# Kernel optimization log

Hardware: AMD Instinct MI355X
Metric: run time of the kernel (lower is better)

## Reference

```python
import jax, jax.numpy as jnp
import numpy as np

N_NODES = 100000
N_EDGES = 600000
N_GRAPHS = 256
HID = 128
IN_DIM = 7
POCKET_DIM = 28
BN_EPS = 1e-5


def setup_inputs() -> dict:
    key = jax.random.key(0)
    ks = jax.random.split(key, 24)
    d = {}
    d['x'] = jax.random.normal(ks[0], (N_NODES, IN_DIM), dtype=jnp.float32)
    d['edge_index'] = jax.random.randint(ks[1], (2, N_EDGES), 0, N_NODES, dtype=jnp.int32)
    d['batch'] = jnp.sort(jax.random.randint(ks[2], (N_NODES,), 0, N_GRAPHS, dtype=jnp.int32))
    d['pocket'] = jax.random.normal(ks[3], (POCKET_DIM,), dtype=jnp.float32)
    # GCN layer weights (PyG GCNConv: lin then normalized aggregation, bias after)
    def glorot(k, shape):
        lim = np.sqrt(6.0 / (shape[0] + shape[1]))
        return jax.random.uniform(k, shape, jnp.float32, -lim, lim)
    d['W0'] = glorot(ks[4], (IN_DIM, HID)); d['b0'] = jnp.zeros((HID,), jnp.float32)
    d['W1'] = glorot(ks[5], (HID, HID)); d['b1'] = jnp.zeros((HID,), jnp.float32)
    d['W2'] = glorot(ks[6], (HID, HID)); d['b2'] = jnp.zeros((HID,), jnp.float32)
    # BatchNorm (eval mode) params for 3 layers
    d['bn_gamma'] = jax.random.uniform(ks[7], (3, HID), jnp.float32, 0.5, 1.5)
    d['bn_beta'] = 0.1 * jax.random.normal(ks[8], (3, HID), dtype=jnp.float32)
    d['bn_mean'] = 0.1 * jax.random.normal(ks[9], (3, HID), dtype=jnp.float32)
    d['bn_var'] = jax.random.uniform(ks[10], (3, HID), jnp.float32, 0.5, 1.5)
    # pocket MLP: 28 -> 64 -> 64
    d['pw1'] = glorot(ks[11], (POCKET_DIM, 64)); d['pb1'] = jnp.zeros((64,), jnp.float32)
    d['pw2'] = glorot(ks[12], (64, 64)); d['pb2'] = jnp.zeros((64,), jnp.float32)
    # classifier: 192 -> 96 -> 1
    d['cw1'] = glorot(ks[13], (HID + 64, 96)); d['cb1'] = jnp.zeros((96,), jnp.float32)
    d['cw2'] = glorot(ks[14], (96, 1)); d['cb2'] = jnp.zeros((1,), jnp.float32)
    return d


def reference(x, edge_index, batch, pocket, W0, b0, W1, b1, W2, b2,
              bn_gamma, bn_beta, bn_mean, bn_var,
              pw1, pb1, pw2, pb2, cw1, cb1, cw2, cb2):
    src, dst = edge_index[0], edge_index[1]
    n = x.shape[0]
    # degree with self-loops (GCNConv default add_self_loops=True)
    deg = jax.ops.segment_sum(jnp.ones((src.shape[0],), x.dtype), dst, num_segments=n) + 1.0
    dinv = jax.lax.rsqrt(deg)                      # [N]
    norm = dinv[src] * dinv[dst]                   # [E] edge normalization
    self_norm = (dinv * dinv)[:, None]             # [N,1] self-loop norm

    h = x
    for i, (W, b) in enumerate(((W0, b0), (W1, b1), (W2, b2))):
        hl = h @ W                                  # [N,HID]
        agg = jax.ops.segment_sum(hl[src] * norm[:, None], dst, num_segments=n)
        agg = agg + hl * self_norm + b
        # BatchNorm1d in eval mode with running stats
        bn = (agg - bn_mean[i]) * (bn_gamma[i] * jax.lax.rsqrt(bn_var[i] + BN_EPS)) + bn_beta[i]
        h = jax.nn.relu(bn)                         # dropout is identity in eval

    # global mean pool over graphs
    sums = jax.ops.segment_sum(h, batch, num_segments=N_GRAPHS)          # [B,HID]
    cnts = jax.ops.segment_sum(jnp.ones((n,), h.dtype), batch, num_segments=N_GRAPHS)
    lig = sums / jnp.maximum(cnts, 1.0)[:, None]

    # pocket MLP, broadcast to batch
    p = jax.nn.relu(pocket @ pw1 + pb1) @ pw2 + pb2                      # [64]
    pe = jnp.broadcast_to(p[None, :], (N_GRAPHS, 64))

    emb = jnp.concatenate([lig, pe], axis=1)                             # [B,192]
    logits = (jax.nn.relu(emb @ cw1 + cb1) @ cw2 + cb2)[:, 0]            # [B]
    return logits
```

## Files before the change

### kernel.cpp

```cpp
#include <hip/hip_runtime.h>

#define NN 100000
#define NE 600000
#define NG 256
#define HID 128
#define BN_EPS 1e-5f

#define SCAN_TILE 1024
#define NTILES ((NN + SCAN_TILE - 1) / SCAN_TILE)
#define MM_TILES (NN / 32)

typedef __attribute__((ext_vector_type(8))) short short8;
typedef __attribute__((ext_vector_type(4))) float float4v;

__device__ __forceinline__ unsigned short f2bf_rn(float f) {
    unsigned u = __float_as_uint(f);
    unsigned r = u + 0x7FFFu + ((u >> 16) & 1u);
    return (unsigned short)(r >> 16);
}
__device__ __forceinline__ float bf2f(unsigned short h) {
    return __uint_as_float((unsigned)h << 16);
}
__device__ __forceinline__ void unpack8(uint4 u, float* f) {
    f[0] = __uint_as_float(u.x << 16); f[1] = __uint_as_float(u.x & 0xFFFF0000u);
    f[2] = __uint_as_float(u.y << 16); f[3] = __uint_as_float(u.y & 0xFFFF0000u);
    f[4] = __uint_as_float(u.z << 16); f[5] = __uint_as_float(u.z & 0xFFFF0000u);
    f[6] = __uint_as_float(u.w << 16); f[7] = __uint_as_float(u.w & 0xFFFF0000u);
}


__global__ __launch_bounds__(256) void hist_kernel(const int* __restrict__ dst, int* __restrict__ cnt) {
    int e = blockIdx.x * blockDim.x + threadIdx.x;
    if (e < NE) atomicAdd(&cnt[dst[e]], 1);
}


__global__ __launch_bounds__(256) void scan_a(const int* __restrict__ cnt, int* __restrict__ rs,
                                              int* __restrict__ tsum, float* __restrict__ dinv) {
    __shared__ int s[256];
    int t = threadIdx.x;
    int base = blockIdx.x * SCAN_TILE;
    int idx = base + t * 4;
    int v0 = (idx + 0 < NN) ? cnt[idx + 0] : 0;
    int v1 = (idx + 1 < NN) ? cnt[idx + 1] : 0;
    int v2 = (idx + 2 < NN) ? cnt[idx + 2] : 0;
    int v3 = (idx + 3 < NN) ? cnt[idx + 3] : 0;
    if (idx + 0 < NN) dinv[idx + 0] = rsqrtf((float)v0 + 1.0f);
    if (idx + 1 < NN) dinv[idx + 1] = rsqrtf((float)v1 + 1.0f);
    if (idx + 2 < NN) dinv[idx + 2] = rsqrtf((float)v2 + 1.0f);
    if (idx + 3 < NN) dinv[idx + 3] = rsqrtf((float)v3 + 1.0f);
    int local = v0 + v1 + v2 + v3;
    s[t] = local;
    __syncthreads();
    for (int off = 1; off < 256; off <<= 1) {
        int x = (t >= off) ? s[t - off] : 0;
        __syncthreads();
        s[t] += x;
        __syncthreads();
    }
    int pre = s[t] - local;
    if (t == 255) tsum[blockIdx.x] = s[255];
    if (idx + 0 < NN) rs[idx + 0] = pre; pre += v0;
    if (idx + 1 < NN) rs[idx + 1] = pre; pre += v1;
    if (idx + 2 < NN) rs[idx + 2] = pre; pre += v2;
    if (idx + 3 < NN) rs[idx + 3] = pre;
}

__global__ __launch_bounds__(128) void scan_b(int* __restrict__ tsum) {
    __shared__ int s[128];
    int t = threadIdx.x;
    int v = (t < NTILES) ? tsum[t] : 0;
    s[t] = v;
    __syncthreads();
    for (int off = 1; off < 128; off <<= 1) {
        int x = (t >= off) ? s[t - off] : 0;
        __syncthreads();
        s[t] += x;
        __syncthreads();
    }
    if (t < NTILES) tsum[t] = s[t] - v;
}

__global__ __launch_bounds__(256) void scan_c(int* __restrict__ rs, const int* __restrict__ tsum,
                                              int* __restrict__ cursor) {
    int t = threadIdx.x;
    int base = blockIdx.x * SCAN_TILE;
    int off = tsum[blockIdx.x];
    for (int k = 0; k < 4; k++) {
        int idx = base + t * 4 + k;
        if (idx < NN) {
            int v = rs[idx] + off;
            rs[idx] = v;
            cursor[idx] = v;
        }
    }
    if (blockIdx.x == 0 && t == 0) rs[NN] = NE;
}


__global__ __launch_bounds__(256) void bucket_prep_kernel(const int* __restrict__ src, const int* __restrict__ dst,
                                                          int* __restrict__ cursor, int* __restrict__ esrc,
                                                          const float* __restrict__ W1, const float* __restrict__ W2,
                                                          unsigned short* __restrict__ w1hi, unsigned short* __restrict__ w1lo,
                                                          unsigned short* __restrict__ w2hi, unsigned short* __restrict__ w2lo,
                                                          const float* __restrict__ pocket,
                                                          const float* __restrict__ pw1, const float* __restrict__ pb1,
                                                          const float* __restrict__ pw2, const float* __restrict__ pb2,
                                                          float* __restrict__ pv, int nb) {
    if ((int)blockIdx.x < nb) {
        int e = blockIdx.x * 256 + threadIdx.x;
        if (e < NE) {
            int pos = atomicAdd(&cursor[dst[e]], 1);
            esrc[pos] = src[e];
        }
    } else if ((int)blockIdx.x < nb + 64) {
        int t = (blockIdx.x - nb) * 256 + threadIdx.x;
        int k = t >> 7, n = t & 127;
        int to = n * HID + k;
        float v1 = W1[t];
        unsigned short h1 = f2bf_rn(v1);
        w1hi[to] = h1;
        w1lo[to] = f2bf_rn(v1 - bf2f(h1));
        float v2 = W2[t];
        unsigned short h2 = f2bf_rn(v2);
        w2hi[to] = h2;
        w2lo[to] = f2bf_rn(v2 - bf2f(h2));
    } else {
        __shared__ float t1[64];
        int j = threadIdx.x;
        if (j < 64) {
            float acc = pb1[j];
            for (int k = 0; k < 28; k++) acc = fmaf(pocket[k], pw1[k * 64 + j], acc);
            t1[j] = fmaxf(acc, 0.f);
        }
        __syncthreads();
        if (j < 64) {
            float acc2 = pb2[j];
            for (int k = 0; k < 64; k++) acc2 = fmaf(t1[k], pw2[k * 64 + j], acc2);
            pv[j] = acc2;
        }
    }
}


__global__ __launch_bounds__(256) void l0_fused(const float* __restrict__ x,
                                                const int* __restrict__ rs,
                                                const int* __restrict__ esrc,
                                                const float* __restrict__ dinv,
                                                const float* __restrict__ W,
                                                const float* __restrict__ b,
                                                const float* __restrict__ gamma,
                                                const float* __restrict__ beta,
                                                const float* __restrict__ mean,
                                                const float* __restrict__ var,
                                                unsigned short* __restrict__ ohi) {
    int c4 = threadIdx.x & 31;
    int r8 = threadIdx.x >> 5;
    float w[7][4];
#pragma unroll
    for (int k = 0; k < 7; k++)
#pragma unroll
        for (int i = 0; i < 4; i++) w[k][i] = W[k * HID + c4 * 4 + i];
    float4 bb = ((const float4*)b)[c4];
    float4 ga = ((const float4*)gamma)[c4];
    float4 be = ((const float4*)beta)[c4];
    float4 me = ((const float4*)mean)[c4];
    float4 va = ((const float4*)var)[c4];
    float4 sc;
    sc.x = ga.x * rsqrtf(va.x + BN_EPS);
    sc.y = ga.y * rsqrtf(va.y + BN_EPS);
    sc.z = ga.z * rsqrtf(va.z + BN_EPS);
    sc.w = ga.w * rsqrtf(va.w + BN_EPS);
    int m = threadIdx.x >> 3, f = threadIdx.x & 7;
    __shared__ float s[32][8];
    int n0 = blockIdx.x * 32;
    float acc = 0.f;
    int n = n0 + m;
    if (f < 7) {
        float di = dinv[n];
        acc = x[n * 7 + f] * di * di;
        int e0 = rs[n], e1 = rs[n + 1];
        int e = e0;
        for (; e + 1 < e1; e += 2) {
            int s0 = esrc[e], s1 = esrc[e + 1];
            float w0 = dinv[s0] * di, w1 = dinv[s1] * di;
            float a0 = x[s0 * 7 + f];
            float a1 = x[s1 * 7 + f];
            acc = fmaf(a0, w0, acc);
            acc = fmaf(a1, w1, acc);
        }
        if (e < e1) {
            int s0 = esrc[e];
            acc = fmaf(x[s0 * 7 + f], dinv[s0] * di, acc);
        }
    }
    s[m][f] = acc;
    __syncthreads();
#pragma unroll
    for (int g = 0; g < 4; g++) {
        int m2 = g * 8 + r8;
        float o0 = bb.x, o1 = bb.y, o2 = bb.z, o3 = bb.w;
#pragma unroll
        for (int k = 0; k < 7; k++) {
            float xv = s[m2][k];
            o0 = fmaf(xv, w[k][0], o0);
            o1 = fmaf(xv, w[k][1], o1);
            o2 = fmaf(xv, w[k][2], o2);
            o3 = fmaf(xv, w[k][3], o3);
        }
        ushort4 hi4;
        hi4.x = f2bf_rn(fmaxf(fmaf(o0 - me.x, sc.x, be.x), 0.f));
        hi4.y = f2bf_rn(fmaxf(fmaf(o1 - me.y, sc.y, be.y), 0.f));
        hi4.z = f2bf_rn(fmaxf(fmaf(o2 - me.z, sc.z, be.z), 0.f));
        hi4.w = f2bf_rn(fmaxf(fmaf(o3 - me.w, sc.w, be.w), 0.f));
        *(ushort4*)(ohi + (size_t)(n0 + m2) * HID + c4 * 4) = hi4;
    }
}


__global__ __launch_bounds__(256) void mm_mfma(const unsigned short* __restrict__ A,
                                               const unsigned short* __restrict__ Whi,
                                               const unsigned short* __restrict__ Wlo,
                                               unsigned short* __restrict__ out) {
    int wave = threadIdx.x >> 6;
    int lane = threadIdx.x & 63;
    int mrow = lane & 15;
    int quad = lane >> 4;
    int n0 = wave * 32;

    short8 bh[2][4], bl[2][4];
#pragma unroll
    for (int ct = 0; ct < 2; ct++) {
#pragma unroll
        for (int kc = 0; kc < 4; kc++) {
            size_t off = (size_t)(n0 + ct * 16 + mrow) * HID + kc * 32 + quad * 8;
            bh[ct][kc] = *(const short8*)(Whi + off);
            bl[ct][kc] = *(const short8*)(Wlo + off);
        }
    }

    int tile = blockIdx.x;
    if (tile >= MM_TILES) return;

    short8 ah[2][4];
#pragma unroll
    for (int rt = 0; rt < 2; rt++)
#pragma unroll
        for (int kc = 0; kc < 4; kc++)
            ah[rt][kc] = *(const short8*)(A + (size_t)(tile * 32 + rt * 16 + mrow) * HID + kc * 32 + quad * 8);

    for (;;) {
        int nt = tile + gridDim.x;
        bool has_next = nt < MM_TILES;
        short8 an[2][4];
        if (has_next) {
#pragma unroll
            for (int rt = 0; rt < 2; rt++)
#pragma unroll
                for (int kc = 0; kc < 4; kc++)
                    an[rt][kc] = *(const short8*)(A + (size_t)(nt * 32 + rt * 16 + mrow) * HID + kc * 32 + quad * 8);
        }

        float4v acc[2][2];
#pragma unroll
        for (int rt = 0; rt < 2; rt++)
#pragma unroll
            for (int ct = 0; ct < 2; ct++) {
                acc[rt][ct].x = 0.f; acc[rt][ct].y = 0.f;
                acc[rt][ct].z = 0.f; acc[rt][ct].w = 0.f;
            }

#pragma unroll
        for (int kc = 0; kc < 4; kc++)
#pragma unroll
            for (int rt = 0; rt < 2; rt++)
#pragma unroll
                for (int ct = 0; ct < 2; ct++) {
                    acc[rt][ct] = __builtin_amdgcn_mfma_f32_16x16x32_bf16(ah[rt][kc], bh[ct][kc], acc[rt][ct], 0, 0, 0);
                    acc[rt][ct] = __builtin_amdgcn_mfma_f32_16x16x32_bf16(ah[rt][kc], bl[ct][kc], acc[rt][ct], 0, 0, 0);
                }

        int m0 = tile * 32;
#pragma unroll
        for (int rt = 0; rt < 2; rt++)
#pragma unroll
            for (int ct = 0; ct < 2; ct++) {
                int col = n0 + ct * 16 + mrow;
#pragma unroll
                for (int r = 0; r < 4; r++) {
                    int row = m0 + rt * 16 + quad * 4 + r;
                    out[(size_t)row * HID + col] = f2bf_rn(acc[rt][ct][r]);
                }
            }

        if (!has_next) break;
#pragma unroll
        for (int rt = 0; rt < 2; rt++)
#pragma unroll
            for (int kc = 0; kc < 4; kc++) ah[rt][kc] = an[rt][kc];
        tile = nt;
    }
}


__global__ __launch_bounds__(256) void gather_bn(const unsigned short* __restrict__ hl,
                                                 const int* __restrict__ rs,
                                                 const int* __restrict__ esrc,
                                                 const float* __restrict__ dinv,
                                                 const float* __restrict__ b,
                                                 const float* __restrict__ gamma,
                                                 const float* __restrict__ beta,
                                                 const float* __restrict__ mean,
                                                 const float* __restrict__ var,
                                                 unsigned short* __restrict__ ohi) {
    int t = blockIdx.x * blockDim.x + threadIdx.x;
    int lane = t & 15;
    int n = t >> 4;
    if (n >= NN) return;
    const uint4* hlv = (const uint4*)hl;
    float di = dinv[n];
    float dsq = di * di;

    float acc[8], v[8];
    {
        uint4 sv = hlv[(size_t)n * 16 + lane];
        unpack8(sv, v);
        float4 bA = ((const float4*)b)[lane * 2];
        float4 bB = ((const float4*)b)[lane * 2 + 1];
        acc[0] = fmaf(v[0], dsq, bA.x); acc[1] = fmaf(v[1], dsq, bA.y);
        acc[2] = fmaf(v[2], dsq, bA.z); acc[3] = fmaf(v[3], dsq, bA.w);
        acc[4] = fmaf(v[4], dsq, bB.x); acc[5] = fmaf(v[5], dsq, bB.y);
        acc[6] = fmaf(v[6], dsq, bB.z); acc[7] = fmaf(v[7], dsq, bB.w);
    }

    int e0 = rs[n], e1 = rs[n + 1];
    int e = e0;
    for (; e + 3 < e1; e += 4) {
        int s0 = esrc[e], s1 = esrc[e + 1], s2 = esrc[e + 2], s3 = esrc[e + 3];
        float w0 = dinv[s0] * di, w1 = dinv[s1] * di;
        float w2 = dinv[s2] * di, w3 = dinv[s3] * di;
        uint4 u0 = hlv[(size_t)s0 * 16 + lane];
        uint4 u1 = hlv[(size_t)s1 * 16 + lane];
        uint4 u2 = hlv[(size_t)s2 * 16 + lane];
        uint4 u3 = hlv[(size_t)s3 * 16 + lane];
        unpack8(u0, v);
#pragma unroll
        for (int i = 0; i < 8; i++) acc[i] = fmaf(v[i], w0, acc[i]);
        unpack8(u1, v);
#pragma unroll
        for (int i = 0; i < 8; i++) acc[i] = fmaf(v[i], w1, acc[i]);
        unpack8(u2, v);
#pragma unroll
        for (int i = 0; i < 8; i++) acc[i] = fmaf(v[i], w2, acc[i]);
        unpack8(u3, v);
#pragma unroll
        for (int i = 0; i < 8; i++) acc[i] = fmaf(v[i], w3, acc[i]);
    }
    for (; e < e1; e++) {
        int s0 = esrc[e];
        float w0 = dinv[s0] * di;
        uint4 u0 = hlv[(size_t)s0 * 16 + lane];
        unpack8(u0, v);
#pragma unroll
        for (int i = 0; i < 8; i++) acc[i] = fmaf(v[i], w0, acc[i]);
    }

    float4 gA = ((const float4*)gamma)[lane * 2], gB = ((const float4*)gamma)[lane * 2 + 1];
    float4 eA = ((const float4*)beta)[lane * 2],  eB = ((const float4*)beta)[lane * 2 + 1];
    float4 mA = ((const float4*)mean)[lane * 2],  mB = ((const float4*)mean)[lane * 2 + 1];
    float4 vA = ((const float4*)var)[lane * 2],   vB = ((const float4*)var)[lane * 2 + 1];
    float o[8];
    o[0] = fmaxf(fmaf(acc[0] - mA.x, gA.x * rsqrtf(vA.x + BN_EPS), eA.x), 0.f);
    o[1] = fmaxf(fmaf(acc[1] - mA.y, gA.y * rsqrtf(vA.y + BN_EPS), eA.y), 0.f);
    o[2] = fmaxf(fmaf(acc[2] - mA.z, gA.z * rsqrtf(vA.z + BN_EPS), eA.z), 0.f);
    o[3] = fmaxf(fmaf(acc[3] - mA.w, gA.w * rsqrtf(vA.w + BN_EPS), eA.w), 0.f);
    o[4] = fmaxf(fmaf(acc[4] - mB.x, gB.x * rsqrtf(vB.x + BN_EPS), eB.x), 0.f);
    o[5] = fmaxf(fmaf(acc[5] - mB.y, gB.y * rsqrtf(vB.y + BN_EPS), eB.y), 0.f);
    o[6] = fmaxf(fmaf(acc[6] - mB.z, gB.z * rsqrtf(vB.z + BN_EPS), eB.z), 0.f);
    o[7] = fmaxf(fmaf(acc[7] - mB.w, gB.w * rsqrtf(vB.w + BN_EPS), eB.w), 0.f);

    uint4 p;
    p.x = (unsigned)f2bf_rn(o[0]) | ((unsigned)f2bf_rn(o[1]) << 16);
    p.y = (unsigned)f2bf_rn(o[2]) | ((unsigned)f2bf_rn(o[3]) << 16);
    p.z = (unsigned)f2bf_rn(o[4]) | ((unsigned)f2bf_rn(o[5]) << 16);
    p.w = (unsigned)f2bf_rn(o[6]) | ((unsigned)f2bf_rn(o[7]) << 16);
    ((uint4*)ohi)[(size_t)n * 16 + lane] = p;
}


__global__ __launch_bounds__(1024) void poolcls_kernel(const unsigned short* __restrict__ h,
                                                       const int* __restrict__ batch,
                                                       const float* __restrict__ pv,
                                                       const float* __restrict__ cw1,
                                                       const float* __restrict__ cb1,
                                                       const float* __restrict__ cw2,
                                                       const float* __restrict__ cb2,
                                                       float* __restrict__ out) {
    int g = blockIdx.x;
    int lane = threadIdx.x & 31;
    int row = threadIdx.x >> 5;
    __shared__ int se[2];
    __shared__ float emb[192];
    __shared__ float hid[96];
    if (threadIdx.x < 2) {
        int target = g + threadIdx.x;
        int lo = 0, hi = NN;
        while (lo < hi) {
            int mid = (lo + hi) >> 1;
            if (batch[mid] < target) lo = mid + 1; else hi = mid;
        }
        se[threadIdx.x] = lo;
    }
    if (threadIdx.x < 64) emb[128 + threadIdx.x] = pv[threadIdx.x];
    __syncthreads();
    int start = se[0], end = se[1];
    const uint2* h2 = (const uint2*)h;
    float4 acc = make_float4(0.f, 0.f, 0.f, 0.f);
    for (int n = start + row; n < end; n += 32) {
        uint2 u = h2[(size_t)n * 32 + lane];
        acc.x += __uint_as_float(u.x << 16);
        acc.y += __uint_as_float(u.x & 0xFFFF0000u);
        acc.z += __uint_as_float(u.y << 16);
        acc.w += __uint_as_float(u.y & 0xFFFF0000u);
    }
    __shared__ float4 part[32][32];
    part[row][lane] = acc;
    __syncthreads();
#pragma unroll
    for (int off = 16; off >= 1; off >>= 1) {
        if (row < off) {
            float4 a = part[row][lane];
            float4 c = part[row + off][lane];
            a.x += c.x; a.y += c.y; a.z += c.z; a.w += c.w;
            part[row][lane] = a;
        }
        __syncthreads();
    }
    if (row == 0) {
        float inv = 1.0f / fmaxf((float)(end - start), 1.0f);
        float4 a = part[0][lane];
        a.x *= inv; a.y *= inv; a.z *= inv; a.w *= inv;
        ((float4*)emb)[lane] = a;
    }
    __syncthreads();
    int j = threadIdx.x;
    if (j < 96) {
        float a = cb1[j];
        for (int k = 0; k < 192; k++) a = fmaf(emb[k], cw1[k * 96 + j], a);
        hid[j] = fmaxf(a, 0.f) * cw2[j];
    }
    __syncthreads();
    if (j == 0) {
        float s = cb2[0];
        for (int k = 0; k < 96; k++) s += hid[k];
        out[g] = s;
    }
}

extern "C" void kernel_launch(void* const* d_in, const int* in_sizes, int n_in,
                              void* d_out, int out_size, void* d_ws, size_t ws_size,
                              hipStream_t stream) {
    const float* x        = (const float*)d_in[0];
    const int*   eidx     = (const int*)d_in[1];
    const int*   batch    = (const int*)d_in[2];
    const float* pocket   = (const float*)d_in[3];
    const float* W0 = (const float*)d_in[4];
    const float* b0 = (const float*)d_in[5];
    const float* W1 = (const float*)d_in[6];
    const float* b1 = (const float*)d_in[7];
    const float* W2 = (const float*)d_in[8];
    const float* b2 = (const float*)d_in[9];
    const float* bn_gamma = (const float*)d_in[10];
    const float* bn_beta  = (const float*)d_in[11];
    const float* bn_mean  = (const float*)d_in[12];
    const float* bn_var   = (const float*)d_in[13];
    const float* pw1 = (const float*)d_in[14]; const float* pb1 = (const float*)d_in[15];
    const float* pw2 = (const float*)d_in[16]; const float* pb2 = (const float*)d_in[17];
    const float* cw1 = (const float*)d_in[18]; const float* cb1 = (const float*)d_in[19];
    const float* cw2 = (const float*)d_in[20]; const float* cb2 = (const float*)d_in[21];
    float* out = (float*)d_out;

    float* ws   = (float*)d_ws;
    float* dinv = ws;
    int*   cnt  = (int*)(ws + NN);
    int*   rs   = cnt + NN;
    int*   tsum = rs + NN + 1;
    int*   esrc = tsum + 128;
    unsigned short* w1hi = (unsigned short*)(esrc + NE);
    unsigned short* w1lo = w1hi + HID * HID;
    unsigned short* w2hi = w1lo + HID * HID;
    unsigned short* w2lo = w2hi + HID * HID;
    size_t head = (size_t)NN * 2 + (NN + 1) + 128 + NE + (4 * HID * HID) / 2;
    head = (head + 3) & ~(size_t)3;
    unsigned short* A = (unsigned short*)(ws + head);
    unsigned short* B = A + (size_t)NN * HID;
    float* pv   = (float*)(B + (size_t)NN * HID);

    const int* srcp = eidx;
    const int* dstp = eidx + NE;

    const int NB = (NE + 255) / 256;

    hipMemsetAsync(cnt, 0, NN * sizeof(int), stream);
    hist_kernel<<<NB, 256, 0, stream>>>(dstp, cnt);
    scan_a<<<NTILES, 256, 0, stream>>>(cnt, rs, tsum, dinv);
    scan_b<<<1, 128, 0, stream>>>(tsum);
    scan_c<<<NTILES, 256, 0, stream>>>(rs, tsum, cnt);
    bucket_prep_kernel<<<NB + 65, 256, 0, stream>>>(srcp, dstp, cnt, esrc,
                                                    W1, W2, w1hi, w1lo, w2hi, w2lo,
                                                    pocket, pw1, pb1, pw2, pb2, pv, NB);

    l0_fused<<<MM_TILES, 256, 0, stream>>>(x, rs, esrc, dinv, W0, b0,
                                           bn_gamma + 0 * HID, bn_beta + 0 * HID,
                                           bn_mean + 0 * HID, bn_var + 0 * HID, A);

    const int MM_BLOCKS = 1024;
    const int GA_BLOCKS = (NN * 16 + 255) / 256;

    mm_mfma<<<MM_BLOCKS, 256, 0, stream>>>(A, w1hi, w1lo, B);
    gather_bn<<<GA_BLOCKS, 256, 0, stream>>>(
        B, rs, esrc, dinv, b1,
        bn_gamma + 1 * HID, bn_beta + 1 * HID, bn_mean + 1 * HID, bn_var + 1 * HID, A);
    mm_mfma<<<MM_BLOCKS, 256, 0, stream>>>(A, w2hi, w2lo, B);
    gather_bn<<<GA_BLOCKS, 256, 0, stream>>>(
        B, rs, esrc, dinv, b2,
        bn_gamma + 2 * HID, bn_beta + 2 * HID, bn_mean + 2 * HID, bn_var + 2 * HID, A);

    poolcls_kernel<<<NG, 1024, 0, stream>>>(A, batch, pv, cw1, cb1, cw2, cb2, out);
}
```

Measured before the change: 334.0 us.

## Sort CSR neighbor lists and order nodes by degree; fold tile scan into scan_c

Adds a degree histogram in scan_a and a degree-bucketed node permutation in scan_c. The separate single-block tile-offset scan is dropped: each scan_c block reduces the earlier tile sums itself. A new kernel uses that permutation to insertion-sort each node's source list, so neighboring threads handle nodes of similar degree. Sorted sources are meant to make the gathers in the aggregation kernels more cache-friendly and deterministic, at the cost of an extra kernel, a wider memset, and extra atomics in the scans.

```diff
diff --git a/kernel.cpp b/kernel.cpp
--- a/kernel.cpp
+++ b/kernel.cpp
@@ -36,8 +36,10 @@
 
 
 __global__ __launch_bounds__(256) void scan_a(const int* __restrict__ cnt, int* __restrict__ rs,
-                                              int* __restrict__ tsum, float* __restrict__ dinv) {
+                                              int* __restrict__ tsum, float* __restrict__ dinv,
+                                              int* __restrict__ dbin) {
     __shared__ int s[256];
+    __shared__ int hb[64];
     int t = threadIdx.x;
     int base = blockIdx.x * SCAN_TILE;
     int idx = base + t * 4;
@@ -51,7 +53,12 @@
     if (idx + 3 < NN) dinv[idx + 3] = rsqrtf((float)v3 + 1.0f);
     int local = v0 + v1 + v2 + v3;
     s[t] = local;
-    __syncthreads();
+    if (t < 64) hb[t] = 0;
+    __syncthreads();
+    if (idx + 0 < NN) atomicAdd(&hb[v0 < 63 ? v0 : 63], 1);
+    if (idx + 1 < NN) atomicAdd(&hb[v1 < 63 ? v1 : 63], 1);
+    if (idx + 2 < NN) atomicAdd(&hb[v2 < 63 ? v2 : 63], 1);
+    if (idx + 3 < NN) atomicAdd(&hb[v3 < 63 ? v3 : 63], 1);
     for (int off = 1; off < 256; off <<= 1) {
         int x = (t >= off) ? s[t - off] : 0;
         __syncthreads();
@@ -60,38 +67,59 @@
     }
     int pre = s[t] - local;
     if (t == 255) tsum[blockIdx.x] = s[255];
+    if (t < 64 && hb[t]) atomicAdd(&dbin[t], hb[t]);
     if (idx + 0 < NN) rs[idx + 0] = pre; pre += v0;
     if (idx + 1 < NN) rs[idx + 1] = pre; pre += v1;
     if (idx + 2 < NN) rs[idx + 2] = pre; pre += v2;
     if (idx + 3 < NN) rs[idx + 3] = pre;
 }
 
-__global__ __launch_bounds__(128) void scan_b(int* __restrict__ tsum) {
-    __shared__ int s[128];
+
+__global__ __launch_bounds__(256) void scan_c(int* __restrict__ rs, const int* __restrict__ tsum,
+                                              int* __restrict__ cursor, const int* __restrict__ dbin,
+                                              int* __restrict__ dcur, int* __restrict__ perm) {
+    __shared__ int s[256];
+    __shared__ int pb[64];
+    __shared__ int lb[64];
     int t = threadIdx.x;
-    int v = (t < NTILES) ? tsum[t] : 0;
-    s[t] = v;
-    __syncthreads();
-    for (int off = 1; off < 128; off <<= 1) {
-        int x = (t >= off) ? s[t - off] : 0;
-        __syncthreads();
-        s[t] += x;
-        __syncthreads();
-    }
-    if (t < NTILES) tsum[t] = s[t] - v;
-}
-
-__global__ __launch_bounds__(256) void scan_c(int* __restrict__ rs, const int* __restrict__ tsum,
-                                              int* __restrict__ cursor) {
-    int t = threadIdx.x;
+    s[t] = (t < (int)blockIdx.x && t < NTILES) ? tsum[t] : 0;
+    if (t < 64) { lb[t] = 0; pb[t] = dbin[t]; }
+    __syncthreads();
+#pragma unroll
+    for (int off = 128; off >= 1; off >>= 1) {
+        if (t < off) s[t] += s[t + off];
+        __syncthreads();
+    }
+    int tile_off = s[0];
+    for (int o = 1; o < 64; o <<= 1) {
+        int x = (t < 64 && t >= o) ? pb[t - o] : 0;
+        __syncthreads();
+        if (t < 64) pb[t] += x;
+        __syncthreads();
+    }
     int base = blockIdx.x * SCAN_TILE;
-    int off = tsum[blockIdx.x];
+    int deg[4], rk[4];
+#pragma unroll
+    for (int k = 0; k < 4; k++) {
+        int idx = base + t * 4 + k;
+        deg[k] = 0; rk[k] = 0;
+        if (idx < NN) {
+            int d = cursor[idx];
+            deg[k] = (d < 63) ? d : 63;
+            rk[k] = atomicAdd(&lb[deg[k]], 1);
+        }
+    }
+    __syncthreads();
+    if (t < 64) lb[t] = (pb[t] - dbin[t]) + atomicAdd(&dcur[t], lb[t]);
+    __syncthreads();
+#pragma unroll
     for (int k = 0; k < 4; k++) {
         int idx = base + t * 4 + k;
         if (idx < NN) {
-            int v = rs[idx] + off;
+            int v = rs[idx] + tile_off;
             rs[idx] = v;
             cursor[idx] = v;
+            perm[lb[deg[k]] + rk[k]] = idx;
         }
     }
     if (blockIdx.x == 0 && t == 0) rs[NN] = NE;
@@ -139,6 +167,22 @@
             for (int k = 0; k < 64; k++) acc2 = fmaf(t1[k], pw2[k * 64 + j], acc2);
             pv[j] = acc2;
         }
+    }
+}
+
+
+__global__ __launch_bounds__(256) void sort_buckets(const int* __restrict__ rs,
+                                                    int* __restrict__ esrc,
+                                                    const int* __restrict__ perm) {
+    int slot = blockIdx.x * 256 + threadIdx.x;
+    if (slot >= NN) return;
+    int n = perm[slot];
+    int e0 = rs[n], e1 = rs[n + 1];
+    for (int i = e0 + 1; i < e1; i++) {
+        int key = esrc[i];
+        int j = i - 1;
+        while (j >= e0 && esrc[j] > key) { esrc[j + 1] = esrc[j]; j--; }
+        esrc[j + 1] = key;
     }
 }
 
@@ -485,12 +529,15 @@
     int*   cnt  = (int*)(ws + NN);
     int*   rs   = cnt + NN;
     int*   tsum = rs + NN + 1;
-    int*   esrc = tsum + 128;
+    int*   dbin = tsum + 128;
+    int*   dcur = dbin + 64;
+    int*   perm = dcur + 64;
+    int*   esrc = perm + NN;
     unsigned short* w1hi = (unsigned short*)(esrc + NE);
     unsigned short* w1lo = w1hi + HID * HID;
     unsigned short* w2hi = w1lo + HID * HID;
     unsigned short* w2lo = w2hi + HID * HID;
-    size_t head = (size_t)NN * 2 + (NN + 1) + 128 + NE + (4 * HID * HID) / 2;
+    size_t head = (size_t)NN * 2 + (NN + 1) + 128 + 64 + 64 + NN + NE + (4 * HID * HID) / 2;
     head = (head + 3) & ~(size_t)3;
     unsigned short* A = (unsigned short*)(ws + head);
     unsigned short* B = A + (size_t)NN * HID;
@@ -501,14 +548,14 @@
 
     const int NB = (NE + 255) / 256;
 
-    hipMemsetAsync(cnt, 0, NN * sizeof(int), stream);
+    hipMemsetAsync(cnt, 0, (size_t)(NN + NN + 1 + 128 + 64 + 64) * sizeof(int), stream);
     hist_kernel<<<NB, 256, 0, stream>>>(dstp, cnt);
-    scan_a<<<NTILES, 256, 0, stream>>>(cnt, rs, tsum, dinv);
-    scan_b<<<1, 128, 0, stream>>>(tsum);
-    scan_c<<<NTILES, 256, 0, stream>>>(rs, tsum, cnt);
+    scan_a<<<NTILES, 256, 0, stream>>>(cnt, rs, tsum, dinv, dbin);
+    scan_c<<<NTILES, 256, 0, stream>>>(rs, tsum, cnt, dbin, dcur, perm);
     bucket_prep_kernel<<<NB + 65, 256, 0, stream>>>(srcp, dstp, cnt, esrc,
                                                     W1, W2, w1hi, w1lo, w2hi, w2lo,
                                                     pocket, pw1, pb1, pw2, pb2, pv, NB);
+    sort_buckets<<<(NN + 255) / 256, 256, 0, stream>>>(rs, esrc, perm);
 
     l0_fused<<<MM_TILES, 256, 0, stream>>>(x, rs, esrc, dinv, W0, b0,
                                            bn_gamma + 0 * HID, bn_beta + 0 * HID,
```

New measurement: 383.1 us. 14.7% more time.
